# Performance work log

Measured on AMD Instinct MI355X. Metric: run time of the kernel, lower is better.

Reference implementation:

```python
import jax, jax.numpy as jnp
import numpy as np

HIDDEN = 512
BATCH = 32
SEQ = 4096


def setup_inputs() -> dict:
    key = jax.random.key(0)
    ks = jax.random.split(key, 8)
    s = 1.0 / np.sqrt(HIDDEN)
    return {
        "encoder_outputs": jax.random.normal(ks[0], (BATCH, SEQ, HIDDEN), jnp.float32),
        "decoder_hidden": jax.random.normal(ks[1], (BATCH, HIDDEN), jnp.float32),
        "W_enc": jax.random.uniform(ks[2], (HIDDEN, HIDDEN), jnp.float32, -s, s),
        "b_enc": jax.random.uniform(ks[3], (HIDDEN,), jnp.float32, -s, s),
        "W_dec": jax.random.uniform(ks[4], (HIDDEN, HIDDEN), jnp.float32, -s, s),
        "b_dec": jax.random.uniform(ks[5], (HIDDEN,), jnp.float32, -s, s),
        "W_v": jax.random.uniform(ks[6], (HIDDEN, 1), jnp.float32, -s, s),
        "b_v": jax.random.uniform(ks[7], (1,), jnp.float32, -s, s),
    }


def reference(encoder_outputs, decoder_hidden, W_enc, b_enc, W_dec, b_dec, W_v, b_v):
    # (b, s, h) projected encoder states
    enc_proj = jnp.einsum("bsh,hk->bsk", encoder_outputs, W_enc) + b_enc
    # (b, 1, h) projected decoder state, broadcast-added over seq
    dec_proj = (decoder_hidden @ W_dec + b_dec)[:, None, :]
    # score: (b, s, 1)
    score = jnp.tanh(enc_proj + dec_proj) @ W_v + b_v
    attention_weights = jax.nn.softmax(score, axis=1)  # softmax over seq_len
    # context: (b, h) weighted sum of encoder outputs
    context = jnp.sum(attention_weights * encoder_outputs, axis=1)
    return context, jnp.squeeze(attention_weights, -1)
```

## Files before the change

kernel.cpp:

```cpp
#include <hip/hip_runtime.h>
#include <hip/hip_bf16.h>

typedef __attribute__((ext_vector_type(8))) short bf16x8;
typedef __attribute__((ext_vector_type(4))) float f32x4;

#define HID 512
#define NB 32
#define SEQL 4096
#define BM 64
#define BK 32
#define NKC 16
#define NBLK 2048

#define WS_BP    0
#define WS_DPROJ (512*1024)
#define WS_SUM   (576*1024)

__device__ __forceinline__ short f2bf(float f) {
    unsigned u = __float_as_uint(f);
    unsigned r = (u + 0x7fffu + ((u >> 16) & 1u)) >> 16;
    return (short)r;
}

__device__ __forceinline__ float fast_tanh(float x) {
    float e = __expf(2.0f * x);
    float r = __builtin_amdgcn_rcpf(e + 1.0f);
    return 1.0f - 2.0f * r;
}

__device__ __forceinline__ void async16(const void* g, void* l) {
    __builtin_amdgcn_global_load_lds((__attribute__((address_space(1))) void*)(g),
                                     (__attribute__((address_space(3))) void*)(l),
                                     16, 0, 0);
}

__global__ void k_pack(const float* __restrict__ W, short* __restrict__ Bp) {
    int tid  = blockIdx.x * 256 + threadIdx.x;
    int lane = tid & 63;
    int nt   = (tid >> 6) & 31;
    int kc   = tid >> 11;
    int k0   = kc * 32 + (lane >> 4) * 8;
    int n    = nt * 16 + (lane & 15);
    bf16x8 v;
#pragma unroll
    for (int j = 0; j < 8; ++j) v[j] = f2bf(W[(size_t)(k0 + j) * HID + n]);
    *(bf16x8*)&Bp[(size_t)tid * 8] = v;
}

__global__ void k_dproj(const float* __restrict__ dec, const float* __restrict__ Wd,
                        const float* __restrict__ be, const float* __restrict__ bd,
                        float* __restrict__ dproj) {
    int t  = threadIdx.x;
    int kl = t & 31, bq = t >> 5;
    int k  = (blockIdx.x & 15) * 32 + kl;
    int b  = (blockIdx.x >> 4) * 8 + bq;
    float a = be[k] + bd[k];
    const float* dr = dec + (size_t)b * HID;
#pragma unroll 8
    for (int h = 0; h < HID; ++h)
        a += dr[h] * Wd[(size_t)h * HID + k];
    dproj[(size_t)b * HID + k] = a;
}

__global__ __launch_bounds__(256, 2)
void k_main(const float* __restrict__ E, const short* __restrict__ Bp,
            const float* __restrict__ dproj, const float* __restrict__ Wv,
            float* __restrict__ out, float* __restrict__ sumacc) {
    __shared__ short As[BM][BK + 8];
    __shared__ short Bs[BK * HID];
    __shared__ float fbuf[640];
    __shared__ float pbuf[BM];

    const int tid  = threadIdx.x;
    const int wave = tid >> 6, lane = tid & 63;
    const int quad = lane >> 4, l15 = lane & 15;
    const int bid  = blockIdx.x;
    const int row0 = bid * BM;
    const int b    = bid >> 6;

    f32x4 acc[4][8];
#pragma unroll
    for (int r = 0; r < 4; ++r)
#pragma unroll
        for (int c = 0; c < 8; ++c) acc[r][c] = (f32x4){0.f, 0.f, 0.f, 0.f};

    const int arow = tid >> 2, akq = tid & 3;
    const float* aptr = E + (size_t)(row0 + arow) * HID + akq * 8;

    for (int kc = 0; kc < NKC; ++kc) {
        float4 a0 = *(const float4*)(aptr + kc * 32);
        float4 a1 = *(const float4*)(aptr + kc * 32 + 4);
        bf16x8 av;
        av[0] = f2bf(a0.x); av[1] = f2bf(a0.y); av[2] = f2bf(a0.z); av[3] = f2bf(a0.w);
        av[4] = f2bf(a1.x); av[5] = f2bf(a1.y); av[6] = f2bf(a1.z); av[7] = f2bf(a1.w);
        *(bf16x8*)&As[arow][akq * 8] = av;
        const short* bsrc = Bp + (size_t)kc * 16384;
#pragma unroll
        for (int i = 0; i < 8; ++i) {
            int off = (i * 4 + wave) * 512;
            async16(bsrc + off + lane * 8, &Bs[off]);
        }
        __syncthreads();
        bf16x8 fa[4];
#pragma unroll
        for (int r = 0; r < 4; ++r) fa[r] = *(bf16x8*)&As[r * 16 + l15][quad * 8];
#pragma unroll
        for (int c = 0; c < 8; ++c) {
            int nt = wave * 8 + c;
            bf16x8 fb = *(bf16x8*)&Bs[(nt * 64 + lane) * 8];
#pragma unroll
            for (int r = 0; r < 4; ++r)
                acc[r][c] = __builtin_amdgcn_mfma_f32_16x16x32_bf16(fa[r], fb, acc[r][c], 0, 0, 0);
        }
        __syncthreads();
    }

    float part[4][4];
#pragma unroll
    for (int r = 0; r < 4; ++r)
#pragma unroll
        for (int g = 0; g < 4; ++g) part[r][g] = 0.f;
    const float* dp = dproj + (size_t)b * HID;
#pragma unroll
    for (int c = 0; c < 8; ++c) {
        int col = wave * 128 + c * 16 + l15;
        float dv = dp[col];
        float wv = Wv[col];
#pragma unroll
        for (int r = 0; r < 4; ++r)
#pragma unroll
            for (int g = 0; g < 4; ++g)
                part[r][g] += fast_tanh(acc[r][c][g] + dv) * wv;
    }
#pragma unroll
    for (int r = 0; r < 4; ++r)
#pragma unroll
        for (int g = 0; g < 4; ++g) {
            float v = part[r][g];
            v += __shfl_xor(v, 1); v += __shfl_xor(v, 2);
            v += __shfl_xor(v, 4); v += __shfl_xor(v, 8);
            part[r][g] = v;
        }
    if (l15 == 0) {
#pragma unroll
        for (int r = 0; r < 4; ++r)
#pragma unroll
            for (int g = 0; g < 4; ++g)
                fbuf[wave * 64 + r * 16 + quad * 4 + g] = part[r][g];
    }
    __syncthreads();
    if (tid < 64) {
        float s  = fbuf[tid] + fbuf[64 + tid] + fbuf[128 + tid] + fbuf[192 + tid];
        float pv = __expf(s);
        pbuf[tid] = pv;
        out[(size_t)NB * HID + row0 + tid] = pv;
        float t2 = pv;
        t2 += __shfl_xor(t2, 1);  t2 += __shfl_xor(t2, 2);  t2 += __shfl_xor(t2, 4);
        t2 += __shfl_xor(t2, 8);  t2 += __shfl_xor(t2, 16); t2 += __shfl_xor(t2, 32);
        if (tid == 0) atomicAdd(&sumacc[b], t2);
    }
    __syncthreads();

    const int hq = tid & 127, rh = tid >> 7;
    const float4* E4 = (const float4*)E;
    size_t cbase = (size_t)(row0 + rh * 32) * (HID / 4) + hq;
    float4 ca = {0.f, 0.f, 0.f, 0.f};
#pragma unroll 4
    for (int rr = 0; rr < 32; ++rr) {
        float w  = pbuf[rh * 32 + rr];
        float4 e = E4[cbase + (size_t)rr * (HID / 4)];
        ca.x += w * e.x; ca.y += w * e.y; ca.z += w * e.z; ca.w += w * e.w;
    }
    if (rh == 1) {
        fbuf[hq] = ca.x; fbuf[128 + hq] = ca.y; fbuf[256 + hq] = ca.z; fbuf[384 + hq] = ca.w;
    }
    __syncthreads();
    if (rh == 0) {
        ca.x += fbuf[hq]; ca.y += fbuf[128 + hq]; ca.z += fbuf[256 + hq]; ca.w += fbuf[384 + hq];
        float* cg = out + (size_t)b * HID + hq * 4;
        atomicAdd(cg + 0, ca.x); atomicAdd(cg + 1, ca.y);
        atomicAdd(cg + 2, ca.z); atomicAdd(cg + 3, ca.w);
    }
}

__global__ void k_finish(float* __restrict__ out, const float* __restrict__ sumacc) {
    int b = blockIdx.x, t = threadIdx.x;
    float rs = 1.0f / sumacc[b];
    for (int i = t; i < HID; i += 256)
        out[(size_t)b * HID + i] *= rs;
    float* ow = out + (size_t)NB * HID + (size_t)b * SEQL;
    for (int i = t; i < SEQL; i += 256)
        ow[i] *= rs;
}

extern "C" void kernel_launch(void* const* d_in, const int* in_sizes, int n_in,
                              void* d_out, int out_size, void* d_ws, size_t ws_size,
                              hipStream_t stream) {
    const float* E   = (const float*)d_in[0];
    const float* dec = (const float*)d_in[1];
    const float* We  = (const float*)d_in[2];
    const float* be  = (const float*)d_in[3];
    const float* Wd  = (const float*)d_in[4];
    const float* bd  = (const float*)d_in[5];
    const float* Wv  = (const float*)d_in[6];
    float* out = (float*)d_out;
    char*  ws  = (char*)d_ws;
    short* Bp     = (short*)(ws + WS_BP);
    float* dproj  = (float*)(ws + WS_DPROJ);
    float* sumacc = (float*)(ws + WS_SUM);

    hipMemsetAsync(out, 0, NB * HID * sizeof(float), stream);
    hipMemsetAsync(sumacc, 0, NB * sizeof(float), stream);
    k_pack<<<128, 256, 0, stream>>>(We, Bp);
    k_dproj<<<64, 256, 0, stream>>>(dec, Wd, be, bd, dproj);
    k_main<<<NBLK, 256, 0, stream>>>(E, Bp, dproj, Wv, out, sumacc);
    k_finish<<<NB, 256, 0, stream>>>(out, sumacc);
}
```

Baseline: 485.3 us.

## Double-buffer GEMM LDS tiles and merge setup kernels into one launch

The main GEMM loop now double-buffers the A and B tiles in LDS. It prefetches the next k-chunk (global loads of E and async copies of packed W) while the MFMAs run on the current chunk, which cuts the loop to one barrier per iteration. The weight-pack, decoder-projection and zeroing of the output and sum buffers are merged into a single pre-kernel, replacing two memsets and two launches. LDS use roughly doubles (about 70KB per block), which may limit the two-blocks-per-CU occupancy target.

```diff
diff --git a/kernel.cpp b/kernel.cpp
--- a/kernel.cpp
+++ b/kernel.cpp
@@ -34,40 +34,46 @@
                                      16, 0, 0);
 }
 
-__global__ void k_pack(const float* __restrict__ W, short* __restrict__ Bp) {
-    int tid  = blockIdx.x * 256 + threadIdx.x;
-    int lane = tid & 63;
-    int nt   = (tid >> 6) & 31;
-    int kc   = tid >> 11;
-    int k0   = kc * 32 + (lane >> 4) * 8;
-    int n    = nt * 16 + (lane & 15);
-    bf16x8 v;
-#pragma unroll
-    for (int j = 0; j < 8; ++j) v[j] = f2bf(W[(size_t)(k0 + j) * HID + n]);
-    *(bf16x8*)&Bp[(size_t)tid * 8] = v;
-}
-
-__global__ void k_dproj(const float* __restrict__ dec, const float* __restrict__ Wd,
-                        const float* __restrict__ be, const float* __restrict__ bd,
-                        float* __restrict__ dproj) {
-    int t  = threadIdx.x;
-    int kl = t & 31, bq = t >> 5;
-    int k  = (blockIdx.x & 15) * 32 + kl;
-    int b  = (blockIdx.x >> 4) * 8 + bq;
-    float a = be[k] + bd[k];
-    const float* dr = dec + (size_t)b * HID;
+__global__ void k_pre(const float* __restrict__ We, short* __restrict__ Bp,
+                      const float* __restrict__ dec, const float* __restrict__ Wd,
+                      const float* __restrict__ be, const float* __restrict__ bd,
+                      float* __restrict__ dproj, float* __restrict__ out,
+                      float* __restrict__ sumacc) {
+    const int blk = blockIdx.x, t = threadIdx.x;
+    if (blk < 128) {
+        int tid  = blk * 256 + t;
+        int lane = tid & 63;
+        int nt   = (tid >> 6) & 31;
+        int kc   = tid >> 11;
+        int k0   = kc * 32 + (lane >> 4) * 8;
+        int n    = nt * 16 + (lane & 15);
+        bf16x8 v;
+#pragma unroll
+        for (int j = 0; j < 8; ++j) v[j] = f2bf(We[(size_t)(k0 + j) * HID + n]);
+        *(bf16x8*)&Bp[(size_t)tid * 8] = v;
+    } else if (blk < 192) {
+        int bid = blk - 128;
+        if (bid == 0 && t < NB) sumacc[t] = 0.f;
+        int kl = t & 31, bq = t >> 5;
+        int k  = (bid & 15) * 32 + kl;
+        int b  = (bid >> 4) * 8 + bq;
+        float a = be[k] + bd[k];
+        const float* dr = dec + (size_t)b * HID;
 #pragma unroll 8
-    for (int h = 0; h < HID; ++h)
-        a += dr[h] * Wd[(size_t)h * HID + k];
-    dproj[(size_t)b * HID + k] = a;
+        for (int h = 0; h < HID; ++h)
+            a += dr[h] * Wd[(size_t)h * HID + k];
+        dproj[(size_t)b * HID + k] = a;
+    } else {
+        out[(blk - 192) * 256 + t] = 0.f;
+    }
 }
 
 __global__ __launch_bounds__(256, 2)
 void k_main(const float* __restrict__ E, const short* __restrict__ Bp,
             const float* __restrict__ dproj, const float* __restrict__ Wv,
             float* __restrict__ out, float* __restrict__ sumacc) {
-    __shared__ short As[BM][BK + 8];
-    __shared__ short Bs[BK * HID];
+    __shared__ short As[2][BM][BK + 8];
+    __shared__ short Bs[2][BK * HID];
     __shared__ float fbuf[640];
     __shared__ float pbuf[BM];
 
@@ -87,32 +93,58 @@
     const int arow = tid >> 2, akq = tid & 3;
     const float* aptr = E + (size_t)(row0 + arow) * HID + akq * 8;
 
-    for (int kc = 0; kc < NKC; ++kc) {
-        float4 a0 = *(const float4*)(aptr + kc * 32);
-        float4 a1 = *(const float4*)(aptr + kc * 32 + 4);
+    {
+        const short* bsrc = Bp;
+#pragma unroll
+        for (int i = 0; i < 8; ++i) {
+            int off = (i * 4 + wave) * 512;
+            async16(bsrc + off + lane * 8, &Bs[0][off]);
+        }
+        float4 a0 = *(const float4*)(aptr);
+        float4 a1 = *(const float4*)(aptr + 4);
         bf16x8 av;
         av[0] = f2bf(a0.x); av[1] = f2bf(a0.y); av[2] = f2bf(a0.z); av[3] = f2bf(a0.w);
         av[4] = f2bf(a1.x); av[5] = f2bf(a1.y); av[6] = f2bf(a1.z); av[7] = f2bf(a1.w);
-        *(bf16x8*)&As[arow][akq * 8] = av;
-        const short* bsrc = Bp + (size_t)kc * 16384;
-#pragma unroll
-        for (int i = 0; i < 8; ++i) {
-            int off = (i * 4 + wave) * 512;
-            async16(bsrc + off + lane * 8, &Bs[off]);
-        }
+        *(bf16x8*)&As[0][arow][akq * 8] = av;
+    }
+
+    int cur = 0;
+    for (int kc = 0; kc < NKC; ++kc) {
+        const int nxt = cur ^ 1;
         __syncthreads();
+
+        float4 a0, a1;
+        const bool pf = (kc + 1 < NKC);
+        if (pf) {
+            a0 = *(const float4*)(aptr + (kc + 1) * 32);
+            a1 = *(const float4*)(aptr + (kc + 1) * 32 + 4);
+            const short* bsrc = Bp + (size_t)(kc + 1) * 16384;
+#pragma unroll
+            for (int i = 0; i < 8; ++i) {
+                int off = (i * 4 + wave) * 512;
+                async16(bsrc + off + lane * 8, &Bs[nxt][off]);
+            }
+        }
+
         bf16x8 fa[4];
 #pragma unroll
-        for (int r = 0; r < 4; ++r) fa[r] = *(bf16x8*)&As[r * 16 + l15][quad * 8];
+        for (int r = 0; r < 4; ++r) fa[r] = *(bf16x8*)&As[cur][r * 16 + l15][quad * 8];
 #pragma unroll
         for (int c = 0; c < 8; ++c) {
             int nt = wave * 8 + c;
-            bf16x8 fb = *(bf16x8*)&Bs[(nt * 64 + lane) * 8];
+            bf16x8 fb = *(bf16x8*)&Bs[cur][(nt * 64 + lane) * 8];
 #pragma unroll
             for (int r = 0; r < 4; ++r)
                 acc[r][c] = __builtin_amdgcn_mfma_f32_16x16x32_bf16(fa[r], fb, acc[r][c], 0, 0, 0);
         }
-        __syncthreads();
+
+        if (pf) {
+            bf16x8 av;
+            av[0] = f2bf(a0.x); av[1] = f2bf(a0.y); av[2] = f2bf(a0.z); av[3] = f2bf(a0.w);
+            av[4] = f2bf(a1.x); av[5] = f2bf(a1.y); av[6] = f2bf(a1.z); av[7] = f2bf(a1.w);
+            *(bf16x8*)&As[nxt][arow][akq * 8] = av;
+        }
+        cur = nxt;
     }
 
     float part[4][4];
@@ -209,10 +241,7 @@
     float* dproj  = (float*)(ws + WS_DPROJ);
     float* sumacc = (float*)(ws + WS_SUM);
 
-    hipMemsetAsync(out, 0, NB * HID * sizeof(float), stream);
-    hipMemsetAsync(sumacc, 0, NB * sizeof(float), stream);
-    k_pack<<<128, 256, 0, stream>>>(We, Bp);
-    k_dproj<<<64, 256, 0, stream>>>(dec, Wd, be, bd, dproj);
+    k_pre<<<256, 256, 0, stream>>>(We, Bp, dec, Wd, be, bd, dproj, out, sumacc);
     k_main<<<NBLK, 256, 0, stream>>>(E, Bp, dproj, Wv, out, sumacc);
     k_finish<<<NB, 256, 0, stream>>>(out, sumacc);
 }
```

After: 492.0 us. Within noise of the previous version (+1.4%).
